# Kernel tuning notes

Hardware: AMD Instinct MI355X
Metric: run time of the kernel (lower is better)

The kernel has to match this reference:

```python
import jax, jax.numpy as jnp
import numpy as np

N, E = 50000, 800000
F_IN, HID, NCLS = 128, 128, 64
EPS = 1e-6


def setup_inputs() -> dict:
    key = jax.random.key(0)
    ks = jax.random.split(key, 6)
    x = jax.random.normal(ks[0], (N, F_IN), dtype=jnp.float32)
    edge_index = jax.random.randint(ks[1], (2, E), 0, N, dtype=jnp.int32)
    # GCNConv glorot init
    W1 = jax.random.normal(ks[2], (F_IN, HID), dtype=jnp.float32) * np.sqrt(2.0 / (F_IN + HID))
    b1 = jnp.zeros((HID,), jnp.float32)
    gamma1 = jnp.ones((HID,), jnp.float32)
    beta1 = jnp.zeros((HID,), jnp.float32)
    W2 = jax.random.normal(ks[3], (HID, NCLS), dtype=jnp.float32) * np.sqrt(2.0 / (HID + NCLS))
    b2 = jnp.zeros((NCLS,), jnp.float32)
    return {"x": x, "edge_index": edge_index, "W1": W1, "b1": b1,
            "gamma1": gamma1, "beta1": beta1, "W2": W2, "b2": b2}


def _gcn_conv(x, src, dst, norm, W, b, n):
    # x' = A_hat @ (x W) + b, A_hat = D^-1/2 (A+I) D^-1/2
    h = x @ W                                   # [N, out]
    msg = h[src] * norm[:, None]                # [E+N, out] gather
    out = jax.ops.segment_sum(msg, dst, num_segments=n)  # scatter-add
    return out + b


def _layer_norm(h, gamma, beta):
    mu = jnp.mean(h, axis=-1, keepdims=True)
    var = jnp.mean(jnp.square(h - mu), axis=-1, keepdims=True)
    return (h - mu) * jax.lax.rsqrt(var + EPS) * gamma + beta


def reference(x, edge_index, W1, b1, gamma1, beta1, W2, b2):
    n = x.shape[0]
    loop = jnp.arange(n, dtype=edge_index.dtype)
    src = jnp.concatenate([edge_index[0], loop])  # add self loops
    dst = jnp.concatenate([edge_index[1], loop])
    deg = jax.ops.segment_sum(jnp.ones_like(dst, jnp.float32), dst, num_segments=n)
    dinv = jnp.where(deg > 0, jax.lax.rsqrt(deg), 0.0)
    norm = dinv[src] * dinv[dst]                 # [E+N]
    h = _gcn_conv(x, src, dst, norm, W1, b1, n)
    h = jax.nn.relu(_layer_norm(h, gamma1, beta1))
    out = _gcn_conv(h, src, dst, norm, W2, b2, n)
    return out
```

## Files before the change

### kernel.cpp

```cpp
#include <hip/hip_runtime.h>


typedef float f32x2 __attribute__((ext_vector_type(2)));
typedef float f32x4 __attribute__((ext_vector_type(4)));
typedef unsigned u32x4 __attribute__((ext_vector_type(4)));
typedef __bf16 bf16x8 __attribute__((ext_vector_type(8)));

__device__ __forceinline__ unsigned short f2bf(float f) {
    unsigned u = __float_as_uint(f);
    u += 0x7FFF + ((u >> 16) & 1);
    return (unsigned short)(u >> 16);
}
__device__ __forceinline__ float bfLo(unsigned g) { return __uint_as_float(g << 16); }
__device__ __forceinline__ float bfHi(unsigned g) { return __uint_as_float(g & 0xFFFF0000u); }

__global__ __launch_bounds__(256) void cvt_wi(const float* __restrict__ W1,
                                              const float* __restrict__ W2,
                                              unsigned short* __restrict__ W1t,
                                              unsigned short* __restrict__ W2t,
                                              int* __restrict__ cnt, int n) {
    int id = blockIdx.x * 256 + threadIdx.x;
    if (id < 128 * 128) {
        int c = id >> 7, k = id & 127;
        W1t[id] = f2bf(W1[k * 128 + c]);
    } else if (id < 128 * 128 + 64 * 128) {
        int j = id - 128 * 128;
        int c = j >> 7, k = j & 127;
        W2t[j] = f2bf(W2[k * 64 + c]);
    }
    if (id < n) cnt[id] = 0;
}

__global__ void count_k(const int* __restrict__ dst, int* __restrict__ cnt,
                        int* __restrict__ rank, int e) {
    int i = blockIdx.x * blockDim.x + threadIdx.x;
    if (i < e) {
        int r = atomicAdd(&cnt[dst[i]], 1);
        __builtin_nontemporal_store(r, &rank[i]);
    }
}

__global__ __launch_bounds__(1024) void scan1_k(const int* __restrict__ cnt,
                                                int* __restrict__ incl,
                                                int* __restrict__ bsum, int n) {
    __shared__ int lds[1024];
    int t = threadIdx.x;
    int i = blockIdx.x * 1024 + t;
    int v = (i < n) ? ((cnt[i] + 7) & ~7) : 0;
    lds[t] = v;
    __syncthreads();
#pragma unroll
    for (int d = 1; d < 1024; d <<= 1) {
        int u = (t >= d) ? lds[t - d] : 0;
        __syncthreads();
        lds[t] += u;
        __syncthreads();
    }
    if (i < n) incl[i] = lds[t];
    if (t == 1023) bsum[blockIdx.x] = lds[1023];
}

__global__ __launch_bounds__(1024) void scan3_k(const int* __restrict__ cnt,
                                                const int* __restrict__ incl,
                                                const int* __restrict__ bsum,
                                                int* __restrict__ offs,
                                                float* __restrict__ dinv,
                                                unsigned* __restrict__ epk,
                                                int nb, int n) {
    __shared__ int sP;
    int t = threadIdx.x, bid = blockIdx.x;
    if (t < 64) {
        int raw = (t < nb) ? bsum[t] : 0;
        int v = raw;
#pragma unroll
        for (int d = 1; d < 64; d <<= 1) {
            int u = __shfl_up(v, d);
            if (t >= d) v += u;
        }
        if (t == bid) sP = v - raw;
    }
    __syncthreads();
    int i = bid * 1024 + t;
    if (i >= n) return;
    int c = cnt[i];
    int c8 = (c + 7) & ~7;
    int inc = sP + incl[i];
    int ex = inc - c8;
    offs[i] = ex;
    dinv[i] = rsqrtf((float)(c + 1));
    for (int j = c; j < c8; ++j)
        __builtin_nontemporal_store(0u, &epk[ex + j]);
    if (i == n - 1) offs[n] = inc;
}

__global__ void fill_k(const int* __restrict__ src, const int* __restrict__ dst,
                       const int* __restrict__ rank, const int* __restrict__ offs,
                       const float* __restrict__ dinv,
                       unsigned* __restrict__ epk, int e) {
    int i = blockIdx.x * blockDim.x + threadIdx.x;
    if (i >= e) return;
    int s = src[i], d = dst[i];
    float w = dinv[s] * dinv[d];
    epk[offs[d] + rank[i]] = ((unsigned)s << 16) | (unsigned)f2bf(w);
}

template<int NT, bool CVT>
__global__ __launch_bounds__(256) void gemm_mfma(const void* __restrict__ Asrc,
                                                 const uint4* __restrict__ Wt,
                                                 unsigned short* __restrict__ tab,
                                                 int n) {
    __shared__ uint4 As[64 * 16];
    int t = threadIdx.x;
    int r0 = blockIdx.x * 64;
    int rows = min(64, n - r0);
#pragma unroll
    for (int it = 0; it < 4; ++it) {
        int u = it * 256 + t;
        int row = u >> 4, s = u & 15;
        uint4 v = make_uint4(0u, 0u, 0u, 0u);
        if (row < rows) {
            if constexpr (CVT) {
                const float4* X4 = (const float4*)Asrc;
                float4 a = X4[(size_t)(r0 + row) * 32 + 2 * s];
                float4 b = X4[(size_t)(r0 + row) * 32 + 2 * s + 1];
                v.x = (unsigned)f2bf(a.x) | ((unsigned)f2bf(a.y) << 16);
                v.y = (unsigned)f2bf(a.z) | ((unsigned)f2bf(a.w) << 16);
                v.z = (unsigned)f2bf(b.x) | ((unsigned)f2bf(b.y) << 16);
                v.w = (unsigned)f2bf(b.z) | ((unsigned)f2bf(b.w) << 16);
            } else {
                v = ((const uint4*)Asrc)[(size_t)(r0 + row) * 16 + s];
            }
        }
        As[row * 16 + (s ^ (row & 7))] = v;
    }
    __syncthreads();

    int wv = t >> 6, lane = t & 63;
    int arow = lane & 15;
    int kg = lane >> 4;
    int lrow = wv * 16 + arow;

    f32x4 acc[NT];
    f32x4 z = {0.f, 0.f, 0.f, 0.f};
#pragma unroll
    for (int j = 0; j < NT; ++j) acc[j] = z;

#pragma unroll
    for (int ks = 0; ks < 4; ++ks) {
        bf16x8 a = __builtin_bit_cast(bf16x8,
                       As[lrow * 16 + ((ks * 4 + kg) ^ (arow & 7))]);
#pragma unroll
        for (int tl = 0; tl < NT; ++tl) {
            bf16x8 b = __builtin_bit_cast(bf16x8,
                           Wt[(size_t)(tl * 16 + arow) * 16 + ks * 4 + kg]);
            acc[tl] = __builtin_amdgcn_mfma_f32_16x16x32_bf16(a, b, acc[tl], 0, 0, 0);
        }
    }

    int grow0 = r0 + wv * 16 + 4 * kg;
#pragma unroll
    for (int r = 0; r < 4; ++r) {
        int grow = grow0 + r;
        if (grow < n) {
            unsigned short* rowp = tab + (size_t)grow * (NT * 16) + arow;
#pragma unroll
            for (int tl = 0; tl < NT; ++tl)
                rowp[tl * 16] = f2bf(acc[tl][r]);
        }
    }
}

__global__ __launch_bounds__(256) void prop_ln(const unsigned* __restrict__ h0b,
                                               const int* __restrict__ offs,
                                               const unsigned* __restrict__ epk,
                                               const float* __restrict__ dinv,
                                               const float* __restrict__ b1,
                                               const float* __restrict__ gamma,
                                               const float* __restrict__ beta,
                                               unsigned* __restrict__ h1b, int n) {
    int wid = __builtin_amdgcn_readfirstlane((blockIdx.x * blockDim.x + threadIdx.x) >> 6);
    int lane = threadIdx.x & 63;
    if (wid >= n) return;
    float di = dinv[wid];
    unsigned self = h0b[(size_t)wid * 64 + lane];
    float a0 = bfLo(self) * di * di;
    float a1 = bfHi(self) * di * di;

    int s0 = offs[wid], s1 = offs[wid + 1];
    if (s0 < s1) {
        const u32x4* ep4 = (const u32x4*)(epk + s0);
        int nb8 = (s1 - s0) >> 3;
        u32x4 d0 = __builtin_nontemporal_load(ep4);
        u32x4 d1 = __builtin_nontemporal_load(ep4 + 1);
        for (int b = 0; b < nb8; ++b) {
            unsigned g0 = h0b[(size_t)(d0.x >> 16) * 64 + lane];
            unsigned g1 = h0b[(size_t)(d0.y >> 16) * 64 + lane];
            unsigned g2 = h0b[(size_t)(d0.z >> 16) * 64 + lane];
            unsigned g3 = h0b[(size_t)(d0.w >> 16) * 64 + lane];
            unsigned g4 = h0b[(size_t)(d1.x >> 16) * 64 + lane];
            unsigned g5 = h0b[(size_t)(d1.y >> 16) * 64 + lane];
            unsigned g6 = h0b[(size_t)(d1.z >> 16) * 64 + lane];
            unsigned g7 = h0b[(size_t)(d1.w >> 16) * 64 + lane];
            float w0 = bfLo(d0.x), w1 = bfLo(d0.y), w2 = bfLo(d0.z), w3 = bfLo(d0.w);
            float w4 = bfLo(d1.x), w5 = bfLo(d1.y), w6 = bfLo(d1.z), w7 = bfLo(d1.w);
            int bn = (b + 1 < nb8) ? b + 1 : 0;
            d0 = __builtin_nontemporal_load(ep4 + 2 * bn);
            d1 = __builtin_nontemporal_load(ep4 + 2 * bn + 1);
            a0 = fmaf(bfLo(g0), w0, a0); a1 = fmaf(bfHi(g0), w0, a1);
            a0 = fmaf(bfLo(g1), w1, a0); a1 = fmaf(bfHi(g1), w1, a1);
            a0 = fmaf(bfLo(g2), w2, a0); a1 = fmaf(bfHi(g2), w2, a1);
            a0 = fmaf(bfLo(g3), w3, a0); a1 = fmaf(bfHi(g3), w3, a1);
            a0 = fmaf(bfLo(g4), w4, a0); a1 = fmaf(bfHi(g4), w4, a1);
            a0 = fmaf(bfLo(g5), w5, a0); a1 = fmaf(bfHi(g5), w5, a1);
            a0 = fmaf(bfLo(g6), w6, a0); a1 = fmaf(bfHi(g6), w6, a1);
            a0 = fmaf(bfLo(g7), w7, a0); a1 = fmaf(bfHi(g7), w7, a1);
        }
    }

    a0 += b1[2 * lane];
    a1 += b1[2 * lane + 1];
    float sum = a0 + a1, sq = a0 * a0 + a1 * a1;
#pragma unroll
    for (int off = 32; off > 0; off >>= 1) {
        sum += __shfl_xor(sum, off);
        sq  += __shfl_xor(sq, off);
    }
    float mu  = sum * (1.f / 128.f);
    float var = fmaxf(sq * (1.f / 128.f) - mu * mu, 0.f);
    float rstd = rsqrtf(var + 1e-6f);
    float y0 = fmaxf((a0 - mu) * rstd * gamma[2 * lane] + beta[2 * lane], 0.f);
    float y1 = fmaxf((a1 - mu) * rstd * gamma[2 * lane + 1] + beta[2 * lane + 1], 0.f);
    unsigned pk = (unsigned)f2bf(y0) | ((unsigned)f2bf(y1) << 16);
    __builtin_nontemporal_store(pk, &h1b[(size_t)wid * 64 + lane]);
}

__global__ __launch_bounds__(256) void prop_out(const unsigned* __restrict__ h2b,
                                                const int* __restrict__ offs,
                                                const unsigned* __restrict__ epk,
                                                const float* __restrict__ dinv,
                                                const float* __restrict__ b2,
                                                float* __restrict__ out, int n) {
    int wid = __builtin_amdgcn_readfirstlane((blockIdx.x * blockDim.x + threadIdx.x) >> 6);
    int lane = threadIdx.x & 63;
    if (wid >= n) return;
    int es = lane >> 5, u = lane & 31;
    float di = dinv[wid];
    float a0 = 0.f, a1 = 0.f;
    if (es == 0) {
        unsigned self = h2b[(size_t)wid * 32 + u];
        a0 = bfLo(self) * di * di;
        a1 = bfHi(self) * di * di;
    }

    int s0 = offs[wid], s1 = offs[wid + 1];
    if (s0 < s1) {
        const u32x4* ep4 = (const u32x4*)(epk + s0);
        int nb8 = (s1 - s0) >> 3;
        u32x4 d0 = __builtin_nontemporal_load(ep4);
        u32x4 d1 = __builtin_nontemporal_load(ep4 + 1);
        for (int b = 0; b < nb8; ++b) {
            unsigned dd0 = es ? d0.y : d0.x;
            unsigned dd1 = es ? d0.w : d0.z;
            unsigned dd2 = es ? d1.y : d1.x;
            unsigned dd3 = es ? d1.w : d1.z;
            unsigned g0 = h2b[(size_t)(dd0 >> 16) * 32 + u];
            unsigned g1 = h2b[(size_t)(dd1 >> 16) * 32 + u];
            unsigned g2 = h2b[(size_t)(dd2 >> 16) * 32 + u];
            unsigned g3 = h2b[(size_t)(dd3 >> 16) * 32 + u];
            float w0 = bfLo(dd0), w1 = bfLo(dd1), w2 = bfLo(dd2), w3 = bfLo(dd3);
            int bn = (b + 1 < nb8) ? b + 1 : 0;
            d0 = __builtin_nontemporal_load(ep4 + 2 * bn);
            d1 = __builtin_nontemporal_load(ep4 + 2 * bn + 1);
            a0 = fmaf(bfLo(g0), w0, a0); a1 = fmaf(bfHi(g0), w0, a1);
            a0 = fmaf(bfLo(g1), w1, a0); a1 = fmaf(bfHi(g1), w1, a1);
            a0 = fmaf(bfLo(g2), w2, a0); a1 = fmaf(bfHi(g2), w2, a1);
            a0 = fmaf(bfLo(g3), w3, a0); a1 = fmaf(bfHi(g3), w3, a1);
        }
    }

    a0 += __shfl_xor(a0, 32);
    a1 += __shfl_xor(a1, 32);
    if (es == 0) {
        f32x2 o; o.x = a0 + b2[2 * u]; o.y = a1 + b2[2 * u + 1];
        __builtin_nontemporal_store(o, &((f32x2*)out)[(size_t)wid * 32 + u]);
    }
}

extern "C" void kernel_launch(void* const* d_in, const int* in_sizes, int n_in,
                              void* d_out, int out_size, void* d_ws, size_t ws_size,
                              hipStream_t stream) {
    const float* x     = (const float*)d_in[0];
    const int*   ei    = (const int*)d_in[1];
    const float* W1    = (const float*)d_in[2];
    const float* b1    = (const float*)d_in[3];
    const float* gam   = (const float*)d_in[4];
    const float* bet   = (const float*)d_in[5];
    const float* W2    = (const float*)d_in[6];
    const float* b2    = (const float*)d_in[7];
    float* out = (float*)d_out;

    int n = in_sizes[0] / 128;
    int e = in_sizes[1] / 2;
    const int* src = ei;
    const int* dst = ei + e;
    size_t ecap = (size_t)e + 8 * (size_t)n;

    char* p = (char*)d_ws;
    auto alloc = [&](size_t bytes) {
        void* q = (void*)p;
        p += (bytes + 255) & ~(size_t)255;
        return q;
    };
    int*            cnt  = (int*)alloc((size_t)n * 4);
    int*            offs = (int*)alloc((size_t)(n + 1) * 4);
    int*            rank = (int*)alloc((size_t)e * 4);
    float*          dinv = (float*)alloc((size_t)n * 4);
    int*            incl = (int*)alloc((size_t)n * 4);
    int*            bsum = (int*)alloc(64 * 4);
    unsigned*       epk  = (unsigned*)alloc(ecap * 4);
    unsigned*       h0b  = (unsigned*)alloc((size_t)n * 64 * 4);
    unsigned*       h1b  = (unsigned*)alloc((size_t)n * 64 * 4);
    unsigned short* W1t  = (unsigned short*)alloc(128 * 128 * 2);
    unsigned short* W2t  = (unsigned short*)alloc(64 * 128 * 2);

    unsigned* h2b = h0b;

    int nb = (n + 1023) / 1024;

    cvt_wi<<<(n + 255) / 256, 256, 0, stream>>>(W1, W2, W1t, W2t, cnt, n);
    count_k<<<(e + 255) / 256, 256, 0, stream>>>(dst, cnt, rank, e);
    scan1_k<<<nb, 1024, 0, stream>>>(cnt, incl, bsum, n);
    scan3_k<<<nb, 1024, 0, stream>>>(cnt, incl, bsum, offs, dinv, epk, nb, n);
    fill_k<<<(e + 255) / 256, 256, 0, stream>>>(src, dst, rank, offs, dinv, epk, e);

    int gb = (n + 63) / 64;
    gemm_mfma<8, true><<<gb, 256, 0, stream>>>(x, (const uint4*)W1t,
                                               (unsigned short*)h0b, n);
    prop_ln<<<(n + 3) / 4, 256, 0, stream>>>(h0b, offs, epk, dinv, b1, gam, bet, h1b, n);
    gemm_mfma<4, false><<<gb, 256, 0, stream>>>(h1b, (const uint4*)W2t,
                                                (unsigned short*)h2b, n);
    prop_out<<<(n + 3) / 4, 256, 0, stream>>>(h2b, offs, epk, dinv, b2, out, n);
}
```

Baseline: 163.7 us.

## Shard layer-1 table into feature slices and move LayerNorm into second GEMM

The first GEMM now writes its bf16 output as four 32-feature column slices, each stored contiguously. The first aggregation processes one slice per block with four edge streams per wave and writes fp32 pre-norm sums. Bias, LayerNorm and ReLU move into the second GEMM's load stage, computed with 16-lane shuffles. The intent is a smaller, more cache-resident gather working set per block, at the cost of an extra fp32 intermediate (twice the bytes of the old bf16 h1) and re-reading the edge list four times.

```diff
diff --git a/kernel.cpp b/kernel.cpp
--- a/kernel.cpp
+++ b/kernel.cpp
@@ -104,10 +104,13 @@
     epk[offs[d] + rank[i]] = ((unsigned)s << 16) | (unsigned)f2bf(w);
 }
 
-template<int NT, bool CVT>
+template<int NT, int MODE, bool SHARD>
 __global__ __launch_bounds__(256) void gemm_mfma(const void* __restrict__ Asrc,
                                                  const uint4* __restrict__ Wt,
                                                  unsigned short* __restrict__ tab,
+                                                 const float* __restrict__ b1,
+                                                 const float* __restrict__ gamma,
+                                                 const float* __restrict__ beta,
                                                  int n) {
     __shared__ uint4 As[64 * 16];
     int t = threadIdx.x;
@@ -119,16 +122,45 @@
         int row = u >> 4, s = u & 15;
         uint4 v = make_uint4(0u, 0u, 0u, 0u);
         if (row < rows) {
-            if constexpr (CVT) {
+            if constexpr (MODE == 0) {
+                v = ((const uint4*)Asrc)[(size_t)(r0 + row) * 16 + s];
+            } else {
                 const float4* X4 = (const float4*)Asrc;
                 float4 a = X4[(size_t)(r0 + row) * 32 + 2 * s];
                 float4 b = X4[(size_t)(r0 + row) * 32 + 2 * s + 1];
+                if constexpr (MODE == 2) {
+                    float4 ba = ((const float4*)b1)[2 * s];
+                    float4 bb = ((const float4*)b1)[2 * s + 1];
+                    a.x += ba.x; a.y += ba.y; a.z += ba.z; a.w += ba.w;
+                    b.x += bb.x; b.y += bb.y; b.z += bb.z; b.w += bb.w;
+                    float sum = a.x + a.y + a.z + a.w + b.x + b.y + b.z + b.w;
+                    float sq = a.x * a.x + a.y * a.y + a.z * a.z + a.w * a.w
+                             + b.x * b.x + b.y * b.y + b.z * b.z + b.w * b.w;
+#pragma unroll
+                    for (int off = 1; off < 16; off <<= 1) {
+                        sum += __shfl_xor(sum, off);
+                        sq  += __shfl_xor(sq, off);
+                    }
+                    float mu = sum * (1.f / 128.f);
+                    float var = fmaxf(sq * (1.f / 128.f) - mu * mu, 0.f);
+                    float rstd = rsqrtf(var + 1e-6f);
+                    float4 ga = ((const float4*)gamma)[2 * s];
+                    float4 gb = ((const float4*)gamma)[2 * s + 1];
+                    float4 ea = ((const float4*)beta)[2 * s];
+                    float4 eb = ((const float4*)beta)[2 * s + 1];
+                    a.x = fmaxf((a.x - mu) * rstd * ga.x + ea.x, 0.f);
+                    a.y = fmaxf((a.y - mu) * rstd * ga.y + ea.y, 0.f);
+                    a.z = fmaxf((a.z - mu) * rstd * ga.z + ea.z, 0.f);
+                    a.w = fmaxf((a.w - mu) * rstd * ga.w + ea.w, 0.f);
+                    b.x = fmaxf((b.x - mu) * rstd * gb.x + eb.x, 0.f);
+                    b.y = fmaxf((b.y - mu) * rstd * gb.y + eb.y, 0.f);
+                    b.z = fmaxf((b.z - mu) * rstd * gb.z + eb.z, 0.f);
+                    b.w = fmaxf((b.w - mu) * rstd * gb.w + eb.w, 0.f);
+                }
                 v.x = (unsigned)f2bf(a.x) | ((unsigned)f2bf(a.y) << 16);
                 v.y = (unsigned)f2bf(a.z) | ((unsigned)f2bf(a.w) << 16);
                 v.z = (unsigned)f2bf(b.x) | ((unsigned)f2bf(b.y) << 16);
                 v.w = (unsigned)f2bf(b.z) | ((unsigned)f2bf(b.w) << 16);
-            } else {
-                v = ((const uint4*)Asrc)[(size_t)(r0 + row) * 16 + s];
             }
         }
         As[row * 16 + (s ^ (row & 7))] = v;
@@ -162,76 +194,62 @@
     for (int r = 0; r < 4; ++r) {
         int grow = grow0 + r;
         if (grow < n) {
-            unsigned short* rowp = tab + (size_t)grow * (NT * 16) + arow;
-#pragma unroll
-            for (int tl = 0; tl < NT; ++tl)
-                rowp[tl * 16] = f2bf(acc[tl][r]);
-        }
-    }
-}
-
-__global__ __launch_bounds__(256) void prop_ln(const unsigned* __restrict__ h0b,
+            if constexpr (SHARD) {
+#pragma unroll
+                for (int tl = 0; tl < NT; ++tl)
+                    tab[(size_t)(tl >> 1) * n * 32 + (size_t)grow * 32 +
+                        ((tl & 1) << 4) + arow] = f2bf(acc[tl][r]);
+            } else {
+                unsigned short* rowp = tab + (size_t)grow * (NT * 16) + arow;
+#pragma unroll
+                for (int tl = 0; tl < NT; ++tl)
+                    rowp[tl * 16] = f2bf(acc[tl][r]);
+            }
+        }
+    }
+}
+
+__global__ __launch_bounds__(256) void prop_g1(const unsigned* __restrict__ tab1,
                                                const int* __restrict__ offs,
                                                const unsigned* __restrict__ epk,
                                                const float* __restrict__ dinv,
-                                               const float* __restrict__ b1,
-                                               const float* __restrict__ gamma,
-                                               const float* __restrict__ beta,
-                                               unsigned* __restrict__ h1b, int n) {
-    int wid = __builtin_amdgcn_readfirstlane((blockIdx.x * blockDim.x + threadIdx.x) >> 6);
+                                               float* __restrict__ h1pre, int n) {
+    int bid = blockIdx.x;
+    int fc = __builtin_amdgcn_readfirstlane(bid & 3);
+    int node = __builtin_amdgcn_readfirstlane((bid >> 2) * 4 + (threadIdx.x >> 6));
+    if (node >= n) return;
     int lane = threadIdx.x & 63;
-    if (wid >= n) return;
-    float di = dinv[wid];
-    unsigned self = h0b[(size_t)wid * 64 + lane];
-    float a0 = bfLo(self) * di * di;
-    float a1 = bfHi(self) * di * di;
-
-    int s0 = offs[wid], s1 = offs[wid + 1];
+    int u = lane & 15, es = lane >> 4;
+    const unsigned* slice = tab1 + (size_t)fc * n * 16;
+    float di = dinv[node];
+    unsigned self = slice[(size_t)node * 16 + u];
+    float a0 = (es == 0) ? bfLo(self) * di * di : 0.f;
+    float a1 = (es == 0) ? bfHi(self) * di * di : 0.f;
+
+    int s0 = offs[node], s1 = offs[node + 1];
     if (s0 < s1) {
-        const u32x4* ep4 = (const u32x4*)(epk + s0);
-        int nb8 = (s1 - s0) >> 3;
-        u32x4 d0 = __builtin_nontemporal_load(ep4);
-        u32x4 d1 = __builtin_nontemporal_load(ep4 + 1);
-        for (int b = 0; b < nb8; ++b) {
-            unsigned g0 = h0b[(size_t)(d0.x >> 16) * 64 + lane];
-            unsigned g1 = h0b[(size_t)(d0.y >> 16) * 64 + lane];
-            unsigned g2 = h0b[(size_t)(d0.z >> 16) * 64 + lane];
-            unsigned g3 = h0b[(size_t)(d0.w >> 16) * 64 + lane];
-            unsigned g4 = h0b[(size_t)(d1.x >> 16) * 64 + lane];
-            unsigned g5 = h0b[(size_t)(d1.y >> 16) * 64 + lane];
-            unsigned g6 = h0b[(size_t)(d1.z >> 16) * 64 + lane];
-            unsigned g7 = h0b[(size_t)(d1.w >> 16) * 64 + lane];
-            float w0 = bfLo(d0.x), w1 = bfLo(d0.y), w2 = bfLo(d0.z), w3 = bfLo(d0.w);
-            float w4 = bfLo(d1.x), w5 = bfLo(d1.y), w6 = bfLo(d1.z), w7 = bfLo(d1.w);
-            int bn = (b + 1 < nb8) ? b + 1 : 0;
-            d0 = __builtin_nontemporal_load(ep4 + 2 * bn);
-            d1 = __builtin_nontemporal_load(ep4 + 2 * bn + 1);
-            a0 = fmaf(bfLo(g0), w0, a0); a1 = fmaf(bfHi(g0), w0, a1);
-            a0 = fmaf(bfLo(g1), w1, a0); a1 = fmaf(bfHi(g1), w1, a1);
-            a0 = fmaf(bfLo(g2), w2, a0); a1 = fmaf(bfHi(g2), w2, a1);
-            a0 = fmaf(bfLo(g3), w3, a0); a1 = fmaf(bfHi(g3), w3, a1);
-            a0 = fmaf(bfLo(g4), w4, a0); a1 = fmaf(bfHi(g4), w4, a1);
-            a0 = fmaf(bfLo(g5), w5, a0); a1 = fmaf(bfHi(g5), w5, a1);
-            a0 = fmaf(bfLo(g6), w6, a0); a1 = fmaf(bfHi(g6), w6, a1);
-            a0 = fmaf(bfLo(g7), w7, a0); a1 = fmaf(bfHi(g7), w7, a1);
-        }
-    }
-
-    a0 += b1[2 * lane];
-    a1 += b1[2 * lane + 1];
-    float sum = a0 + a1, sq = a0 * a0 + a1 * a1;
-#pragma unroll
-    for (int off = 32; off > 0; off >>= 1) {
-        sum += __shfl_xor(sum, off);
-        sq  += __shfl_xor(sq, off);
-    }
-    float mu  = sum * (1.f / 128.f);
-    float var = fmaxf(sq * (1.f / 128.f) - mu * mu, 0.f);
-    float rstd = rsqrtf(var + 1e-6f);
-    float y0 = fmaxf((a0 - mu) * rstd * gamma[2 * lane] + beta[2 * lane], 0.f);
-    float y1 = fmaxf((a1 - mu) * rstd * gamma[2 * lane + 1] + beta[2 * lane + 1], 0.f);
-    unsigned pk = (unsigned)f2bf(y0) | ((unsigned)f2bf(y1) << 16);
-    __builtin_nontemporal_store(pk, &h1b[(size_t)wid * 64 + lane]);
+        int k = s0;
+        unsigned dA = __builtin_nontemporal_load(&epk[k + es]);
+        unsigned dB = __builtin_nontemporal_load(&epk[k + 4 + es]);
+        while (k < s1) {
+            unsigned gA = slice[(size_t)(dA >> 16) * 16 + u];
+            unsigned gB = slice[(size_t)(dB >> 16) * 16 + u];
+            float wA = bfLo(dA), wB = bfLo(dB);
+            k += 8;
+            int kn = (k < s1) ? k : s0;
+            dA = __builtin_nontemporal_load(&epk[kn + es]);
+            dB = __builtin_nontemporal_load(&epk[kn + 4 + es]);
+            a0 = fmaf(bfLo(gA), wA, a0); a1 = fmaf(bfHi(gA), wA, a1);
+            a0 = fmaf(bfLo(gB), wB, a0); a1 = fmaf(bfHi(gB), wB, a1);
+        }
+    }
+    a0 += __shfl_xor(a0, 16); a1 += __shfl_xor(a1, 16);
+    a0 += __shfl_xor(a0, 32); a1 += __shfl_xor(a1, 32);
+    if (es == 0) {
+        f32x2 o; o.x = a0; o.y = a1;
+        __builtin_nontemporal_store(o,
+            &((f32x2*)h1pre)[(size_t)node * 64 + fc * 16 + u]);
+    }
 }
 
 __global__ __launch_bounds__(256) void prop_out(const unsigned* __restrict__ h2b,
@@ -311,19 +329,19 @@
         p += (bytes + 255) & ~(size_t)255;
         return q;
     };
-    int*            cnt  = (int*)alloc((size_t)n * 4);
-    int*            offs = (int*)alloc((size_t)(n + 1) * 4);
-    int*            rank = (int*)alloc((size_t)e * 4);
-    float*          dinv = (float*)alloc((size_t)n * 4);
-    int*            incl = (int*)alloc((size_t)n * 4);
-    int*            bsum = (int*)alloc(64 * 4);
-    unsigned*       epk  = (unsigned*)alloc(ecap * 4);
-    unsigned*       h0b  = (unsigned*)alloc((size_t)n * 64 * 4);
-    unsigned*       h1b  = (unsigned*)alloc((size_t)n * 64 * 4);
-    unsigned short* W1t  = (unsigned short*)alloc(128 * 128 * 2);
-    unsigned short* W2t  = (unsigned short*)alloc(64 * 128 * 2);
-
-    unsigned* h2b = h0b;
+    int*            cnt   = (int*)alloc((size_t)n * 4);
+    int*            offs  = (int*)alloc((size_t)(n + 1) * 4);
+    int*            rank  = (int*)alloc((size_t)e * 4);
+    float*          dinv  = (float*)alloc((size_t)n * 4);
+    int*            incl  = (int*)alloc((size_t)n * 4);
+    int*            bsum  = (int*)alloc(64 * 4);
+    unsigned*       epk   = (unsigned*)alloc(ecap * 4);
+    unsigned*       tab1  = (unsigned*)alloc((size_t)n * 64 * 4);
+    float*          h1pre = (float*)alloc((size_t)n * 128 * 4);
+    unsigned short* W1t   = (unsigned short*)alloc(128 * 128 * 2);
+    unsigned short* W2t   = (unsigned short*)alloc(64 * 128 * 2);
+
+    unsigned* h2b = tab1;
 
     int nb = (n + 1023) / 1024;
 
@@ -334,10 +352,11 @@
     fill_k<<<(e + 255) / 256, 256, 0, stream>>>(src, dst, rank, offs, dinv, epk, e);
 
     int gb = (n + 63) / 64;
-    gemm_mfma<8, true><<<gb, 256, 0, stream>>>(x, (const uint4*)W1t,
-                                               (unsigned short*)h0b, n);
-    prop_ln<<<(n + 3) / 4, 256, 0, stream>>>(h0b, offs, epk, dinv, b1, gam, bet, h1b, n);
-    gemm_mfma<4, false><<<gb, 256, 0, stream>>>(h1b, (const uint4*)W2t,
-                                                (unsigned short*)h2b, n);
+    int pb1 = ((n + 3) / 4) * 4;
+    gemm_mfma<8, 1, true><<<gb, 256, 0, stream>>>(
+        x, (const uint4*)W1t, (unsigned short*)tab1, nullptr, nullptr, nullptr, n);
+    prop_g1<<<pb1, 256, 0, stream>>>(tab1, offs, epk, dinv, h1pre, n);
+    gemm_mfma<4, 2, false><<<gb, 256, 0, stream>>>(
+        h1pre, (const uint4*)W2t, (unsigned short*)h2b, b1, gam, bet, n);
     prop_out<<<(n + 3) / 4, 256, 0, stream>>>(h2b, offs, epk, dinv, b2, out, n);
 }
```

New measurement: 216.2 us. +32.0%, slower.
